# Optimization experiments

Measured on AMD Instinct MI355X. Metric: run time of the kernel, lower is better.

The kernel has to match this reference:

```python
import jax, jax.numpy as jnp
import numpy as np

HEADS, DIM_HEAD, LANDMARKS, PINV_ITERS = 8, 64, 256, 6


def moore_penrose_pinv(x, iters=PINV_ITERS):
    abs_x = jnp.abs(x)
    col = abs_x.sum(-1)
    row = abs_x.sum(-2)
    z = jnp.swapaxes(x, -1, -2) / (jnp.max(col) * jnp.max(row))
    I = jnp.eye(x.shape[-1], dtype=x.dtype)
    for _ in range(iters):
        xz = x @ z
        z = 0.25 * z @ (13 * I - xz @ (15 * I - xz @ (7 * I - xz)))
    return z


def nystrom_attention(x, w_qkv, w_out, b_out, res_conv_w):
    b, n, dim = x.shape
    m = LANDMARKS
    pad = (m - n % m) % m
    x = jnp.pad(x, ((0, 0), (pad, 0), (0, 0)))  # pad at front like F.pad(x,(0,0,pad,0))
    npad = n + pad
    qkv = x @ w_qkv  # (b, npad, 3*heads*dim_head)
    q, k, v = jnp.split(qkv, 3, axis=-1)
    sh = lambda t: t.reshape(b, npad, HEADS, DIM_HEAD).transpose(0, 2, 1, 3)
    q, k, v = sh(q), sh(k), sh(v)  # (b,h,npad,dh)
    q = q * (DIM_HEAD ** -0.5)
    l = npad // m
    q_l = q.reshape(b, HEADS, m, l, DIM_HEAD).mean(axis=3)  # landmarks (b,h,m,dh)
    k_l = k.reshape(b, HEADS, m, l, DIM_HEAD).mean(axis=3)
    attn1 = jax.nn.softmax(jnp.einsum('bhid,bhjd->bhij', q, k_l), -1)   # (b,h,npad,m)
    attn2 = jax.nn.softmax(jnp.einsum('bhid,bhjd->bhij', q_l, k_l), -1)  # (b,h,m,m)
    attn3 = jax.nn.softmax(jnp.einsum('bhid,bhjd->bhij', q_l, k), -1)   # (b,h,m,npad)
    out = attn1 @ (moore_penrose_pinv(attn2) @ (attn3 @ v))  # (b,h,npad,dh)
    # depthwise residual conv over sequence dim (Conv2d(heads,heads,(33,1),groups=heads,bias=False))
    res = jax.lax.conv_general_dilated(v, res_conv_w, (1, 1), ((16, 16), (0, 0)),
                                       dimension_numbers=('NCHW', 'OIHW', 'NCHW'),
                                       feature_group_count=HEADS)
    out = out + res
    out = out.transpose(0, 2, 1, 3).reshape(b, npad, HEADS * DIM_HEAD)
    out = out @ w_out + b_out
    return out[:, -n:]


def camil_forward(bag, adj_row, adj_col, adj_val, w_qkv, w_out, b_out, res_conv_w,
                  wq, wk, wv_w, wv_b, v_att, u_att, w_att, fc_kernel, fc_bias):
    N = bag.shape[1]
    # encoder
    xg = nystrom_attention(bag, w_qkv, w_out, b_out, res_conv_w)[0]  # (N,D)
    enc = xg + bag  # (1,N,D)
    q = enc @ wq  # (1,N,256)
    k = enc @ wk
    attn = jnp.einsum('bnd,bmd->bnm', q, k)[0] / jnp.sqrt(jnp.float32(256.0))  # (N,N)
    # sparse adjacency-masked neighbor aggregation
    edge_scores = adj_val * attn[adj_row, adj_col]
    A_raw = jax.ops.segment_sum(edge_scores, adj_row, num_segments=N)  # (N,)
    alpha = jax.nn.softmax(A_raw)
    value = bag @ wv_w + wv_b  # (1,N,D)
    xl = alpha[:, None] * value  # (1,N,D)
    wei2 = jax.nn.sigmoid(-xl) ** 2
    xo = xl * 2 * wei2 + 2 * enc * (1 - wei2)  # (1,N,D)
    # gated MIL attention (softmax over dim 0 of size 1, as in original)
    inst = jnp.tanh(xo @ v_att) * jax.nn.sigmoid(xo @ u_att)
    scores = inst @ w_att  # (1,N,1)
    k_alpha = jax.nn.softmax(scores, axis=0)
    attn_output = k_alpha * xo
    pooled = attn_output[0].sum(axis=0, keepdims=True)  # (1,D)
    out = pooled @ fc_kernel + fc_bias  # (1,1)
    return out, A_raw, k_alpha


def setup_inputs() -> dict:
    key = jax.random.key(0)
    ks = jax.random.split(key, 16)
    N, D, E = 10000, 512, 90000
    s = 0.02
    return {
        'bag': jax.random.normal(ks[0], (1, N, D), jnp.float32),
        'adj_row': jax.random.randint(ks[1], (E,), 0, N),
        'adj_col': jax.random.randint(ks[2], (E,), 0, N),
        'adj_val': jax.random.uniform(ks[3], (E,), jnp.float32),
        'w_qkv': jax.random.normal(ks[4], (D, 3 * HEADS * DIM_HEAD), jnp.float32) * s,
        'w_out': jax.random.normal(ks[5], (HEADS * DIM_HEAD, D), jnp.float32) * s,
        'b_out': jnp.zeros((D,), jnp.float32),
        'res_conv_w': jax.random.normal(ks[6], (HEADS, 1, 33, 1), jnp.float32) * s,
        'wq': jax.random.normal(ks[7], (D, 256), jnp.float32) * s,
        'wk': jax.random.normal(ks[8], (D, 256), jnp.float32) * s,
        'wv_w': jax.random.normal(ks[9], (D, D), jnp.float32) * s,
        'wv_b': jnp.zeros((D,), jnp.float32),
        'v_att': jax.random.normal(ks[10], (D, 128), jnp.float32) * s,
        'u_att': jax.random.normal(ks[11], (D, 128), jnp.float32) * s,
        'w_att': jax.random.normal(ks[12], (128, 1), jnp.float32) * s,
        'fc_kernel': jax.random.normal(ks[13], (D, 1), jnp.float32) * s,
        'fc_bias': jnp.zeros((1,), jnp.float32),
    }


def reference(bag, adj_row, adj_col, adj_val, w_qkv, w_out, b_out, res_conv_w,
              wq, wk, wv_w, wv_b, v_att, u_att, w_att, fc_kernel, fc_bias):
    return camil_forward(bag, adj_row, adj_col, adj_val, w_qkv, w_out, b_out, res_conv_w,
                         wq, wk, wv_w, wv_b, v_att, u_att, w_att, fc_kernel, fc_bias)
```

## Files before the change

### kernel.cpp

```cpp
#include <hip/hip_runtime.h>
#include <hip/hip_bf16.h>
#include <math.h>

#define NSEQ   10000
#define NPAD   10240
#define PADR   240
#define HEADS  8
#define DH     64
#define LM     256
#define LFAC   40
#define DMODEL 512
#define DQK    256
#define OUTSZ  20001
#define NSPLIT 16
#define KCH    128

typedef __attribute__((ext_vector_type(8))) short bf16x8;
typedef __attribute__((ext_vector_type(4))) float f32x4;
#define MFMA16(a,b,c) __builtin_amdgcn_mfma_f32_16x16x32_bf16(a,b,c,0,0,0)

__device__ __forceinline__ float b2f(ushort u) {
    return __uint_as_float(((unsigned)u) << 16);
}
__device__ __forceinline__ ushort f2b(float f) {
    unsigned u = __float_as_uint(f);
    unsigned r = (u + 0x7FFFu + ((u >> 16) & 1u)) >> 16;
    return (ushort)r;
}
__device__ __forceinline__ int swz8(int bid, int nwg) {
    int q = nwg >> 3, r = nwg & 7;
    int x = bid & 7, idx = bid >> 3;
    int start = (x < r) ? x * (q + 1) : r * (q + 1) + (x - r) * q;
    return start + idx;
}

__global__ __launch_bounds__(256) void cvt_k(const float* __restrict__ in,
                                             ushort* __restrict__ out, int n4)
{
    int i = blockIdx.x * 256 + threadIdx.x;
    if (i < n4) {
        float4 v = ((const float4*)in)[i];
        ushort4 u; u.x = f2b(v.x); u.y = f2b(v.y); u.z = f2b(v.z); u.w = f2b(v.w);
        ((ushort4*)out)[i] = u;
    }
}

__global__ __launch_bounds__(256)
void wtrans_k(const float* __restrict__ w_qkv, const float* __restrict__ w_out,
              const float* __restrict__ wq, const float* __restrict__ wk,
              const float* __restrict__ wv_w,
              ushort* __restrict__ wqkvT, ushort* __restrict__ woutT,
              ushort* __restrict__ wqkT)
{
    __shared__ float tile[32][33];
    int g0 = blockIdx.x * 32, r0 = blockIdx.y * 32;
    const float* in; ushort* outp; int C; int lc0;
    if (g0 < 1536)      { in = w_qkv; outp = wqkvT;                      C = 1536; lc0 = g0; }
    else if (g0 < 2048) { in = w_out; outp = woutT;                      C = 512;  lc0 = g0 - 1536; }
    else if (g0 < 2304) { in = wq;    outp = wqkT;                       C = 256;  lc0 = g0 - 2048; }
    else if (g0 < 2560) { in = wk;    outp = wqkT + 256*512;             C = 256;  lc0 = g0 - 2304; }
    else                { in = wv_w;  outp = wqkvT + (size_t)1536*512;   C = 512;  lc0 = g0 - 2560; }
    int tx = threadIdx.x & 31, ty = threadIdx.x >> 5;
    for (int i = ty; i < 32; i += 8) tile[i][tx] = in[(size_t)(r0 + i) * C + lc0 + tx];
    __syncthreads();
    for (int i = ty; i < 32; i += 8) outp[(size_t)(lc0 + i) * 512 + r0 + tx] = f2b(tile[tx][i]);
}

template<int MODE, int TN>
__global__ __launch_bounds__(256)
void mgemm(const ushort* __restrict__ A, const ushort* __restrict__ Bt,
           int Mlog, int N, int K, int padr, int nbx,
           void* __restrict__ P0, void* __restrict__ P1, void* __restrict__ P2,
           void* __restrict__ P3, void* __restrict__ P4,
           const float* __restrict__ bias, const float* __restrict__ extra)
{
    constexpr int NF = TN / 32;
    __shared__ ushort As[128 * 40];
    __shared__ ushort Bs[TN * 40];
    const int tid = threadIdx.x;
    const int l = tid & 63, w = tid >> 6;
    const int wm = w >> 1, wn = w & 1;
    const int wk_ = swz8(blockIdx.x, gridDim.x);
    const int row0 = (wk_ / nbx) * 128, col0 = (wk_ % nbx) * TN;
    const int lr = l & 15, lk = (l >> 4) * 8;
    const int lg = l >> 4;
    f32x4 acc[4][NF];
    #pragma unroll
    for (int i = 0; i < 4; ++i)
        #pragma unroll
        for (int j = 0; j < NF; ++j) acc[i][j] = (f32x4){0.f, 0.f, 0.f, 0.f};

    for (int k0 = 0; k0 < K; k0 += 32) {
        {
            int row = tid >> 1, half = (tid & 1) * 16;
            int phys = row0 + row - padr;
            uint4 v0 = {0,0,0,0}, v1 = {0,0,0,0};
            if (phys >= 0 && phys < Mlog - padr) {
                const uint4* src = (const uint4*)(A + (size_t)phys * K + k0 + half);
                v0 = src[0]; v1 = src[1];
            }
            *(uint4*)&As[row * 40 + half] = v0;
            *(uint4*)&As[row * 40 + half + 8] = v1;
        }
        if (TN == 128) {
            int row = tid >> 1, half = (tid & 1) * 16;
            const uint4* src = (const uint4*)(Bt + (size_t)(col0 + row) * K + k0 + half);
            *(uint4*)&Bs[row * 40 + half] = src[0];
            *(uint4*)&Bs[row * 40 + half + 8] = src[1];
        } else {
            int row = tid >> 2, q8 = (tid & 3) * 8;
            *(uint4*)&Bs[row * 40 + q8] =
                *(const uint4*)(Bt + (size_t)(col0 + row) * K + k0 + q8);
        }
        __syncthreads();
        bf16x8 af[4];
        #pragma unroll
        for (int mf = 0; mf < 4; ++mf)
            af[mf] = *(const bf16x8*)&As[(wm * 64 + mf * 16 + lr) * 40 + lk];
        #pragma unroll
        for (int nf = 0; nf < NF; ++nf) {
            bf16x8 bfr = *(const bf16x8*)&Bs[(wn * (TN / 2) + nf * 16 + lr) * 40 + lk];
            #pragma unroll
            for (int mf = 0; mf < 4; ++mf)
                acc[mf][nf] = MFMA16(af[mf], bfr, acc[mf][nf]);
        }
        __syncthreads();
    }

    #pragma unroll
    for (int mf = 0; mf < 4; ++mf)
    #pragma unroll
    for (int nf = 0; nf < NF; ++nf) {
        #pragma unroll
        for (int i = 0; i < 4; ++i) {
            int r = row0 + wm * 64 + mf * 16 + lg * 4 + i;
            int c = col0 + wn * (TN / 2) + nf * 16 + lr;
            float v = acc[mf][nf][i];
            if (MODE == 0) {
                int t = c >> 9;
                if (t < 3) {
                    int hh = (c >> 6) & 7, d = c & 63;
                    ushort* dst = (t == 0) ? (ushort*)P0 : (t == 1) ? (ushort*)P1 : (ushort*)P2;
                    dst[((size_t)hh * NPAD + r) * DH + d] = f2b(t == 0 ? v * 0.125f : v);
                } else {
                    int phys = r - PADR;
                    if (phys >= 0)
                        ((ushort*)P4)[(size_t)phys * DMODEL + (c & 511)] = f2b(v);
                }
            } else if (MODE == 1) {
                if (r < Mlog) {
                    float o = v + bias[c] + extra[(size_t)r * N + c];
                    ((float*)P0)[(size_t)r * N + c] = o;
                    ((ushort*)P1)[(size_t)r * N + c] = f2b(o);
                }
            } else if (MODE == 6) {
                if (r < Mlog) {
                    ushort u = f2b(v);
                    if (c < 256) ((ushort*)P0)[(size_t)r * 256 + c] = u;
                    else         ((ushort*)P1)[(size_t)r * 256 + (c - 256)] = u;
                }
            }
        }
        if (MODE == 0) {
            int c = col0 + wn * (TN / 2) + nf * 16 + lr;
            if ((c >> 9) == 2) {
                int hh = (c >> 6) & 7;
                int kt  = (row0 + wm * 64 + mf * 16 + lg * 4) >> 5;
                int lgp = ((mf * 2) + (lg >> 1)) & 3;
                int lanep = lr + lgp * 16;
                int e0 = (lg & 1) * 4;
                ushort4 pk;
                pk.x = f2b(acc[mf][nf][0]); pk.y = f2b(acc[mf][nf][1]);
                pk.z = f2b(acc[mf][nf][2]); pk.w = f2b(acc[mf][nf][3]);
                *(ushort4*)&((ushort*)P3)[(((size_t)hh * (NPAD/32) + kt) * 4 + (nf & 3)) * 512
                                          + lanep * 8 + e0] = pk;
            }
        }
    }
}

template<bool PLAIN, bool BCI>
__global__ __launch_bounds__(256)
void pinv_k(const ushort* __restrict__ A, const ushort* __restrict__ Bt,
            int N, float cval, float scale,
            ushort* __restrict__ P0, ushort* __restrict__ P1)
{
    __shared__ __align__(16) char smem[65536];
    char* As = smem;
    char* Bs = smem + 32768;
    const int tid = threadIdx.x, l = tid & 63, w = tid >> 6;
    const int wm = w >> 1, wn = w & 1;
    const int lr = l & 15, lg = l >> 4;
    const int col0 = blockIdx.x * 64, row0 = blockIdx.y * 64, h = blockIdx.z;
    const ushort* Ab = A + (size_t)h * 65536;
    const ushort* Btb = Bt + (size_t)h * ((size_t)N * 256);
    {
        int row = tid >> 2, seg = (tid & 3) * 128;
        const uint4* sa = (const uint4*)(Ab + (size_t)(row0 + row) * 256) + (tid & 3) * 8;
        const uint4* sb = (const uint4*)(Btb + (size_t)(col0 + row) * 256) + (tid & 3) * 8;
        int gn = col0 + row;
        #pragma unroll
        for (int e = 0; e < 8; ++e) {
            int off = (row * 512 + seg + e * 16) ^ ((row & 7) << 4);
            *(uint4*)(As + off) = sa[e];
            uint4 vb = sb[e];
            if (BCI) {
                union { uint4 u; ushort s[8]; } t; t.u = vb;
                int gk0 = (seg >> 1) + e * 8;
                #pragma unroll
                for (int j = 0; j < 8; ++j)
                    t.s[j] = f2b(((gn == gk0 + j) ? cval : 0.f) - b2f(t.s[j]));
                vb = t.u;
            }
            *(uint4*)(Bs + off) = vb;
        }
    }
    __syncthreads();
    f32x4 acc[2][2];
    #pragma unroll
    for (int i = 0; i < 2; ++i)
        #pragma unroll
        for (int j = 0; j < 2; ++j) acc[i][j] = (f32x4){0.f, 0.f, 0.f, 0.f};
    #pragma unroll
    for (int ks = 0; ks < 8; ++ks) {
        bf16x8 af[2], bf[2];
        #pragma unroll
        for (int mf = 0; mf < 2; ++mf) {
            int ar = wm * 32 + mf * 16 + lr;
            af[mf] = *(const bf16x8*)(As + ((ar * 512 + ks * 64 + lg * 16) ^ ((ar & 7) << 4)));
        }
        #pragma unroll
        for (int nf = 0; nf < 2; ++nf) {
            int br = wn * 32 + nf * 16 + lr;
            bf[nf] = *(const bf16x8*)(Bs + ((br * 512 + ks * 64 + lg * 16) ^ ((br & 7) << 4)));
        }
        #pragma unroll
        for (int mf = 0; mf < 2; ++mf)
            #pragma unroll
            for (int nf = 0; nf < 2; ++nf)
                acc[mf][nf] = MFMA16(af[mf], bf[nf], acc[mf][nf]);
    }
    #pragma unroll
    for (int mf = 0; mf < 2; ++mf)
    #pragma unroll
    for (int nf = 0; nf < 2; ++nf) {
        int r0v = row0 + wm * 32 + mf * 16 + lg * 4;
        int c = col0 + wn * 32 + nf * 16 + lr;
        if (PLAIN) {
            #pragma unroll
            for (int i = 0; i < 4; ++i)
                P0[(size_t)h * 256 * N + (size_t)(r0v + i) * N + c] = f2b(acc[mf][nf][i] * scale);
        }
        ushort4 pk;
        pk.x = f2b(acc[mf][nf][0] * scale); pk.y = f2b(acc[mf][nf][1] * scale);
        pk.z = f2b(acc[mf][nf][2] * scale); pk.w = f2b(acc[mf][nf][3] * scale);
        *(ushort4*)&P1[(size_t)h * ((size_t)N * 256) + (size_t)c * 256 + r0v] = pk;
    }
}

__global__ void landmark_k(const ushort* __restrict__ src, ushort* __restrict__ dst,
                           ushort* __restrict__ dstp)
{
    int b = blockIdx.x;
    int hh = b >> 8, j = b & 255, d = threadIdx.x;
    const ushort* p = src + ((size_t)hh * NPAD + (size_t)j * LFAC) * DH + d;
    float s = 0.f;
    #pragma unroll
    for (int t = 0; t < LFAC; ++t) s += b2f(p[t * DH]);
    ushort u = f2b(s * (1.f / LFAC));
    dst[((size_t)hh * LM + j) * DH + d] = u;
    if (dstp) {
        int nf = j >> 4, lr = j & 15;
        int ks = d >> 5, lg = (d >> 3) & 3, e = d & 7;
        dstp[(((size_t)hh * 16 + nf) * 2 + ks) * 512 + (lg * 16 + lr) * 8 + e] = u;
    }
}

__global__ __launch_bounds__(256)
void wpack_k(const ushort* __restrict__ WT, ushort* __restrict__ Wpk)
{
    int h = blockIdx.x;
    for (int it = 0; it < 8; ++it) {
        int idx = it * 256 + threadIdx.x;
        int nf = idx >> 9, ks = (idx >> 6) & 7, l = idx & 63;
        int lr = l & 15, lg = l >> 4;
        uint4 v = *(const uint4*)(WT + ((size_t)h * 64 + nf * 16 + lr) * 256 + ks * 32 + lg * 8);
        *(uint4*)(Wpk + ((size_t)h * 2048 + idx) * 8) = v;
    }
}

__global__ __launch_bounds__(256)
void attn2_k(const ushort* __restrict__ QL, const ushort* __restrict__ KL,
             ushort* __restrict__ X2b)
{
    int i = blockIdx.x, h = blockIdx.y, j = threadIdx.x;
    __shared__ float qv[DH];
    __shared__ float red[256];
    if (j < DH) qv[j] = b2f(QL[((size_t)h * LM + i) * DH + j]);
    __syncthreads();
    const ushort* kp = KL + ((size_t)h * LM + j) * DH;
    float dot = 0.f;
    #pragma unroll
    for (int d = 0; d < DH; ++d) dot += qv[d] * b2f(kp[d]);
    red[j] = dot; __syncthreads();
    for (int s = 128; s > 0; s >>= 1) { if (j < s) red[j] = fmaxf(red[j], red[j + s]); __syncthreads(); }
    float mx = red[0]; __syncthreads();
    float e = __expf(dot - mx);
    red[j] = e; __syncthreads();
    for (int s = 128; s > 0; s >>= 1) { if (j < s) red[j] += red[j + s]; __syncthreads(); }
    X2b[((size_t)h * LM + i) * LM + j] = f2b(e / red[0]);
}

__global__ __launch_bounds__(256)
void colrow_k(const ushort* __restrict__ X2b, unsigned int* __restrict__ mx)
{
    int h = blockIdx.x, t = threadIdx.x;
    const ushort* x = X2b + (size_t)h * LM * LM;
    float cs = 0.f, rs = 0.f;
    for (int j = 0; j < LM; ++j) cs += fabsf(b2f(x[(size_t)t * LM + j]));
    for (int i = 0; i < LM; ++i) rs += fabsf(b2f(x[(size_t)i * LM + t]));
    __shared__ float r1[256], r2[256];
    r1[t] = cs; r2[t] = rs; __syncthreads();
    for (int s = 128; s > 0; s >>= 1) {
        if (t < s) { r1[t] = fmaxf(r1[t], r1[t + s]); r2[t] = fmaxf(r2[t], r2[t + s]); }
        __syncthreads();
    }
    if (t == 0) {
        atomicMax(&mx[0], __float_as_uint(r1[0]));
        atomicMax(&mx[1], __float_as_uint(r2[0]));
    }
}

__global__ void zinit_k(const ushort* __restrict__ X2b, const float* __restrict__ mxf,
                        ushort* __restrict__ Z, ushort* __restrict__ Zt)
{
    int i = blockIdx.x, h = blockIdx.y, j = threadIdx.x;
    float scale = 1.f / (mxf[0] * mxf[1]);
    float x = b2f(X2b[((size_t)h * LM + i) * LM + j]) * scale;
    ushort u = f2b(x);
    Z[((size_t)h * LM + j) * LM + i] = u;
    Zt[((size_t)h * LM + i) * LM + j] = u;
}

__global__ __launch_bounds__(256)
void attn3_fa(const ushort* __restrict__ QLb, const ushort* __restrict__ Kb,
              const ushort* __restrict__ VtPk,
              float* __restrict__ Opart, float* __restrict__ Mpart,
              float* __restrict__ Lpart)
{
    __shared__ __align__(16) char smem[9216 + 18432];
    ushort* Qs = (ushort*)smem;
    ushort* Ks = (ushort*)(smem + 9216);
    ushort* Ps = (ushort*)(smem + 9216);
    const int tid = threadIdx.x, l = tid & 63, wv = tid >> 6;
    const int split = blockIdx.x, qt = blockIdx.y, h = blockIdx.z;
    const int lr = l & 15, lg = l >> 4;
    {
        int row = tid >> 2, seg = (tid & 3) * 16;
        const uint4* src = (const uint4*)(QLb + ((size_t)h * LM + qt * 64 + row) * DH + seg);
        *(uint4*)&Qs[row * 72 + seg] = src[0];
        *(uint4*)&Qs[row * 72 + seg + 8] = src[1];
    }
    f32x4 o[4];
    float m_[4], l_[4];
    #pragma unroll
    for (int nf = 0; nf < 4; ++nf) o[nf] = (f32x4){0.f, 0.f, 0.f, 0.f};
    #pragma unroll
    for (int i = 0; i < 4; ++i) { m_[i] = -INFINITY; l_[i] = 0.f; }
    const int k0base = split * (NPAD / NSPLIT);
    for (int ch = 0; ch < NPAD / NSPLIT / KCH; ++ch) {
        int kg0 = k0base + ch * KCH;
        __syncthreads();
        {
            int row = tid >> 1, half = (tid & 1) * 32;
            const uint4* src = (const uint4*)(Kb + ((size_t)h * NPAD + kg0 + row) * DH + half);
            #pragma unroll
            for (int e = 0; e < 4; ++e) *(uint4*)&Ks[row * 72 + half + e * 8] = src[e];
        }
        __syncthreads();
        f32x4 s[8];
        #pragma unroll
        for (int nf = 0; nf < 8; ++nf) s[nf] = (f32x4){0.f, 0.f, 0.f, 0.f};
        #pragma unroll
        for (int ks = 0; ks < 2; ++ks) {
            bf16x8 a = *(const bf16x8*)&Qs[(wv * 16 + lr) * 72 + ks * 32 + lg * 8];
            #pragma unroll
            for (int nf = 0; nf < 8; ++nf) {
                bf16x8 b = *(const bf16x8*)&Ks[(nf * 16 + lr) * 72 + ks * 32 + lg * 8];
                s[nf] = MFMA16(a, b, s[nf]);
            }
        }
        float scl[4];
        #pragma unroll
        for (int i = 0; i < 4; ++i) {
            float mx = s[0][i];
            #pragma unroll
            for (int nf = 1; nf < 8; ++nf) mx = fmaxf(mx, s[nf][i]);
            mx = fmaxf(mx, __shfl_xor(mx, 1)); mx = fmaxf(mx, __shfl_xor(mx, 2));
            mx = fmaxf(mx, __shfl_xor(mx, 4)); mx = fmaxf(mx, __shfl_xor(mx, 8));
            float mn = fmaxf(m_[i], mx);
            float sum = 0.f;
            #pragma unroll
            for (int nf = 0; nf < 8; ++nf) {
                float e = __expf(s[nf][i] - mn); s[nf][i] = e; sum += e;
            }
            sum += __shfl_xor(sum, 1); sum += __shfl_xor(sum, 2);
            sum += __shfl_xor(sum, 4); sum += __shfl_xor(sum, 8);
            float sc = __expf(m_[i] - mn);
            l_[i] = l_[i] * sc + sum;
            m_[i] = mn;
            scl[i] = sc;
        }
        #pragma unroll
        for (int nf = 0; nf < 4; ++nf)
        #pragma unroll
        for (int i = 0; i < 4; ++i) o[nf][i] *= scl[i];
        __syncthreads();
        #pragma unroll
        for (int nf = 0; nf < 8; ++nf)
        #pragma unroll
        for (int i = 0; i < 4; ++i) {
            int row = wv * 16 + lg * 4 + i;
            int col = nf * 16 + lr;
            Ps[row * 128 + (col ^ ((row & 7) << 3))] = f2b(s[nf][i]);
        }
        #pragma unroll
        for (int ks = 0; ks < 4; ++ks) {
            int row = wv * 16 + lr;
            int kcol = ks * 32 + lg * 8;
            bf16x8 a = *(const bf16x8*)&Ps[row * 128 + (kcol ^ ((row & 7) << 3))];
            int kgt = (kg0 >> 5) + ks;
            #pragma unroll
            for (int nf = 0; nf < 4; ++nf) {
                bf16x8 b = *(const bf16x8*)(VtPk +
                    (((size_t)h * (NPAD/32) + kgt) * 4 + nf) * 512 + (size_t)l * 8);
                o[nf] = MFMA16(a, b, o[nf]);
            }
        }
    }
    const int base = (split * 4 + qt) * 8 + h;
    #pragma unroll
    for (int nf = 0; nf < 4; ++nf)
    #pragma unroll
    for (int i = 0; i < 4; ++i) {
        int r = wv * 16 + lg * 4 + i;
        int c = nf * 16 + lr;
        Opart[((size_t)base * 64 + r) * 64 + c] = o[nf][i];
    }
    if (lr == 0) {
        #pragma unroll
        for (int i = 0; i < 4; ++i) {
            int r = wv * 16 + lg * 4 + i;
            Mpart[base * 64 + r] = m_[i];
            Lpart[base * 64 + r] = l_[i];
        }
    }
}

__global__ __launch_bounds__(256)
void mergeAV_k(const float* __restrict__ Opart, const float* __restrict__ Mpart,
               const float* __restrict__ Lpart, ushort* __restrict__ AVt)
{
    int qt = blockIdx.x, h = blockIdx.y, rq = blockIdx.z;
    int t = threadIdx.x;
    int r = rq * 32 + (t >> 3), c0 = (t & 7) * 8;
    float mv[NSPLIT];
    float mstar = -INFINITY;
    #pragma unroll
    for (int s = 0; s < NSPLIT; ++s) {
        mv[s] = Mpart[((s * 4 + qt) * 8 + h) * 64 + r];
        mstar = fmaxf(mstar, mv[s]);
    }
    float wgt[NSPLIT];
    float L = 0.f;
    #pragma unroll
    for (int s = 0; s < NSPLIT; ++s) {
        wgt[s] = __expf(mv[s] - mstar);
        L += wgt[s] * Lpart[((s * 4 + qt) * 8 + h) * 64 + r];
    }
    float inv = 1.f / L;
    float acc[8] = {};
    #pragma unroll
    for (int s = 0; s < NSPLIT; ++s) {
        const float* op = Opart + (((size_t)(s * 4 + qt) * 8 + h) * 64 + r) * 64 + c0;
        #pragma unroll
        for (int e = 0; e < 8; ++e) acc[e] += wgt[s] * op[e];
    }
    #pragma unroll
    for (int e = 0; e < 8; ++e)
        AVt[((size_t)h * DH + c0 + e) * LM + qt * 64 + r] = f2b(acc[e] * inv);
}

__global__ __launch_bounds__(256)
void conv_k(const ushort* __restrict__ Vb, const float* __restrict__ cw,
            ushort* __restrict__ OBc)
{
    int idx = blockIdx.x * 256 + threadIdx.x;
    if (idx >= NSEQ * 128) return;
    int ro = idx >> 7, c4 = idx & 127;
    int h = c4 >> 4, dq = (c4 & 15) * 4;
    int i = ro + PADR;
    float a0 = 0, a1 = 0, a2 = 0, a3 = 0;
    #pragma unroll
    for (int tt = 0; tt < 33; ++tt) {
        int src = i + tt - 16;
        if (src < NPAD) {
            float wv = cw[h * 33 + tt];
            ushort4 u = *(const ushort4*)(Vb + ((size_t)h * NPAD + src) * DH + dq);
            a0 += wv * b2f(u.x); a1 += wv * b2f(u.y);
            a2 += wv * b2f(u.z); a3 += wv * b2f(u.w);
        }
    }
    ushort4 o; o.x = f2b(a0); o.y = f2b(a1); o.z = f2b(a2); o.w = f2b(a3);
    *(ushort4*)&OBc[(size_t)ro * DMODEL + h * DH + dq] = o;
}

__global__ __launch_bounds__(256, 4)
void outrows64v2(const ushort* __restrict__ Qb, const ushort* __restrict__ KLpk,
                 const ushort* __restrict__ Wpk, const ushort* __restrict__ OBc,
                 ushort* __restrict__ OBb)
{
    __shared__ __align__(16) char smem[40960];
    char*   Qs  = smem;
    ushort* KLs = (ushort*)(smem + 8192);
    ushort* Ps  = (ushort*)(smem + 8192);
    const int tid = threadIdx.x, l = tid & 63, w = tid >> 6;
    const int h = blockIdx.y, i0 = blockIdx.x * 64;
    const int lr = l & 15, lg = l >> 4;

    ushort obc[4][4];
    #pragma unroll
    for (int nf = 0; nf < 4; ++nf)
    #pragma unroll
    for (int i = 0; i < 4; ++i) {
        int r = i0 + w * 16 + lg * 4 + i;
        obc[nf][i] = (r >= PADR)
            ? OBc[(size_t)(r - PADR) * DMODEL + h * DH + nf * 16 + lr] : (ushort)0;
    }
    {
        int row = tid >> 2;
        int seg = (tid & 3) * 32;
        const uint4* src = (const uint4*)(Qb + ((size_t)h * NPAD + i0 + row) * DH) + (tid & 3) * 2;
        uint4 v0 = src[0], v1 = src[1];
        int sw = (row & 7) << 4;
        *(uint4*)(Qs + row * 128 + (seg ^ sw)) = v0;
        *(uint4*)(Qs + row * 128 + ((seg + 16) ^ sw)) = v1;
    }
    {
        const uint4* src = (const uint4*)(KLpk + (size_t)h * 16384) + tid;
        uint4* dst = (uint4*)KLs + tid;
        #pragma unroll
        for (int e = 0; e < 8; ++e) dst[e * 256] = src[e * 256];
    }
    __syncthreads();

    f32x4 s[16];
    #pragma unroll
    for (int nf = 0; nf < 16; ++nf) s[nf] = (f32x4){0.f, 0.f, 0.f, 0.f};
    #pragma unroll
    for (int ks = 0; ks < 2; ++ks) {
        int qrow = w * 16 + lr;
        bf16x8 a = *(const bf16x8*)(Qs + qrow * 128 +
                                    ((ks * 64 + lg * 16) ^ ((qrow & 7) << 4)));
        #pragma unroll
        for (int nf = 0; nf < 16; ++nf) {
            bf16x8 b = *(const bf16x8*)&KLs[((nf * 2 + ks) * 64 + l) * 8];
            s[nf] = MFMA16(a, b, s[nf]);
        }
    }
    float inv_[4];
    #pragma unroll
    for (int i = 0; i < 4; ++i) {
        float m = s[0][i];
        #pragma unroll
        for (int nf = 1; nf < 16; ++nf) m = fmaxf(m, s[nf][i]);
        m = fmaxf(m, __shfl_xor(m, 1)); m = fmaxf(m, __shfl_xor(m, 2));
        m = fmaxf(m, __shfl_xor(m, 4)); m = fmaxf(m, __shfl_xor(m, 8));
        float sum = 0.f;
        #pragma unroll
        for (int nf = 0; nf < 16; ++nf) {
            float e = __expf(s[nf][i] - m); s[nf][i] = e; sum += e;
        }
        sum += __shfl_xor(sum, 1); sum += __shfl_xor(sum, 2);
        sum += __shfl_xor(sum, 4); sum += __shfl_xor(sum, 8);
        inv_[i] = 1.f / sum;
    }
    __syncthreads();
    #pragma unroll
    for (int nf = 0; nf < 16; ++nf)
    #pragma unroll
    for (int i = 0; i < 4; ++i) {
        int row = w * 16 + lg * 4 + i;
        int col = nf * 16 + lr;
        Ps[row * 256 + (col ^ ((row & 7) << 3))] = f2b(s[nf][i] * inv_[i]);
    }
    f32x4 o[4];
    #pragma unroll
    for (int nf = 0; nf < 4; ++nf) o[nf] = (f32x4){0.f, 0.f, 0.f, 0.f};
    #pragma unroll
    for (int ks = 0; ks < 8; ++ks) {
        int row = w * 16 + lr;
        int kcol = ks * 32 + lg * 8;
        bf16x8 a = *(const bf16x8*)&Ps[row * 256 + (kcol ^ ((row & 7) << 3))];
        #pragma unroll
        for (int nf = 0; nf < 4; ++nf) {
            bf16x8 b = *(const bf16x8*)(Wpk + (((size_t)h * 2048) + nf * 512 + ks * 64 + l) * 8);
            o[nf] = MFMA16(a, b, o[nf]);
        }
    }
    #pragma unroll
    for (int nf = 0; nf < 4; ++nf)
    #pragma unroll
    for (int i = 0; i < 4; ++i) {
        int r = i0 + w * 16 + lg * 4 + i;
        if (r >= PADR) {
            int ro = r - PADR;
            int c = h * DH + nf * 16 + lr;
            OBb[(size_t)ro * DMODEL + c] = f2b(o[nf][i] + b2f(obc[nf][i]));
        }
    }
}

__global__ __launch_bounds__(256)
void edges_k(const int* __restrict__ rows, const int* __restrict__ cols,
             const float* __restrict__ vals,
             const ushort* __restrict__ QE, const ushort* __restrict__ KE,
             float* __restrict__ A_raw, int E)
{
    int gid = blockIdx.x * blockDim.x + threadIdx.x;
    int e = gid >> 6, l = gid & 63;
    if (e >= E) return;
    int r = rows[e], c = cols[e];
    ushort4 qv = *(const ushort4*)(QE + (size_t)r * DQK + l * 4);
    ushort4 kv = *(const ushort4*)(KE + (size_t)c * DQK + l * 4);
    float dot = b2f(qv.x) * b2f(kv.x) + b2f(qv.y) * b2f(kv.y)
              + b2f(qv.z) * b2f(kv.z) + b2f(qv.w) * b2f(kv.w);
    #pragma unroll
    for (int s = 32; s > 0; s >>= 1) dot += __shfl_down(dot, s);
    if (l == 0) atomicAdd(&A_raw[r], vals[e] * dot * 0.0625f);
}

__global__ __launch_bounds__(1024)
void alphasm_k(const float* __restrict__ A_raw, float* __restrict__ alpha)
{
    __shared__ float red[1024];
    int t = threadIdx.x;
    float lm = -INFINITY;
    for (int i = t; i < NSEQ; i += 1024) lm = fmaxf(lm, A_raw[i]);
    red[t] = lm; __syncthreads();
    for (int s = 512; s > 0; s >>= 1) { if (t < s) red[t] = fmaxf(red[t], red[t + s]); __syncthreads(); }
    float mx = red[0]; __syncthreads();
    float ls = 0.f;
    for (int i = t; i < NSEQ; i += 1024) ls += __expf(A_raw[i] - mx);
    red[t] = ls; __syncthreads();
    for (int s = 512; s > 0; s >>= 1) { if (t < s) red[t] += red[t + s]; __syncthreads(); }
    float inv = 1.f / red[0];
    for (int i = t; i < NSEQ; i += 1024) alpha[i] = __expf(A_raw[i] - mx) * inv;
}

__global__ void init_k(float* __restrict__ out, const float* __restrict__ fcb,
                       unsigned int* __restrict__ mx)
{
    int t = blockIdx.x * blockDim.x + threadIdx.x;
    if (t == 0) { out[0] = fcb[0]; mx[0] = 0u; mx[1] = 0u; }
    if (t >= 1 && t <= NSEQ) out[t] = 0.f;
    if (t >= NSEQ + 1 && t < OUTSZ) out[t] = 1.0f;
}

__global__ __launch_bounds__(256)
void xo_pooled_k(const ushort* __restrict__ VALb, const float* __restrict__ ENCf,
                 const float* __restrict__ alpha, const float* __restrict__ wvb,
                 const float* __restrict__ fck, float* __restrict__ out0)
{
    __shared__ float red[256];
    int t = threadIdx.x;
    float acc = 0.f;
    const int total = NSEQ * 128;
    for (int idx = blockIdx.x * 256 + t; idx < total; idx += gridDim.x * 256) {
        int r = idx >> 7, dq = (idx & 127) * 4;
        float al = alpha[r];
        ushort4 v4 = *(const ushort4*)(VALb + (size_t)r * DMODEL + dq);
        float4 e4 = *(const float4*)(ENCf + (size_t)r * DMODEL + dq);
        float4 b4 = *(const float4*)(wvb + dq);
        float4 f4 = *(const float4*)(fck + dq);
        float vv[4] = {b2f(v4.x) + b4.x, b2f(v4.y) + b4.y,
                       b2f(v4.z) + b4.z, b2f(v4.w) + b4.w};
        float ee[4] = {e4.x, e4.y, e4.z, e4.w};
        float ff[4] = {f4.x, f4.y, f4.z, f4.w};
        #pragma unroll
        for (int j = 0; j < 4; ++j) {
            float xl = al * vv[j];
            float s = 1.f / (1.f + __expf(xl));
            float w2 = s * s;
            float xo = 2.f * xl * w2 + 2.f * ee[j] * (1.f - w2);
            acc += xo * ff[j];
        }
    }
    red[t] = acc; __syncthreads();
    for (int s = 128; s > 0; s >>= 1) { if (t < s) red[t] += red[t + s]; __syncthreads(); }
    if (t == 0) atomicAdd(out0, red[0]);
}

extern "C" void kernel_launch(void* const* d_in, const int* in_sizes, int n_in,
                              void* d_out, int out_size, void* d_ws, size_t ws_size,
                              hipStream_t stream)
{
    (void)n_in; (void)out_size; (void)ws_size;
    const float* bag   = (const float*)d_in[0];
    const int*   arow  = (const int*)d_in[1];
    const int*   acol  = (const int*)d_in[2];
    const float* aval  = (const float*)d_in[3];
    const float* w_qkv = (const float*)d_in[4];
    const float* w_out = (const float*)d_in[5];
    const float* b_out = (const float*)d_in[6];
    const float* convw = (const float*)d_in[7];
    const float* wq    = (const float*)d_in[8];
    const float* wk    = (const float*)d_in[9];
    const float* wv_w  = (const float*)d_in[10];
    const float* wv_b  = (const float*)d_in[11];
    const float* fck   = (const float*)d_in[15];
    const float* fcb   = (const float*)d_in[16];
    const int E = in_sizes[1];
    float* out = (float*)d_out;

    char* ws = (char*)d_ws;
    size_t off = 0;
    auto alloc = [&](size_t bytes) { void* p = ws + off; off += (bytes + 255) & ~(size_t)255; return p; };
    ushort* Qb    = (ushort*)alloc((size_t)HEADS * NPAD * DH * 2);
    ushort* Kb    = (ushort*)alloc((size_t)HEADS * NPAD * DH * 2);
    ushort* Vb    = (ushort*)alloc((size_t)HEADS * NPAD * DH * 2);
    ushort* bagb  = (ushort*)alloc((size_t)NSEQ * DMODEL * 2);
    ushort* wqkvT = (ushort*)alloc((size_t)2048 * 512 * 2);
    ushort* woutT = (ushort*)alloc((size_t)512 * 512 * 2);
    ushort* wqkT  = (ushort*)alloc((size_t)512 * 512 * 2);
    ushort* VALb  = (ushort*)alloc((size_t)NSEQ * DMODEL * 2);
    ushort* QLb   = (ushort*)alloc((size_t)HEADS * LM * DH * 2);
    ushort* KLb   = (ushort*)alloc((size_t)HEADS * LM * DH * 2);
    ushort* KLpk  = (ushort*)alloc((size_t)HEADS * LM * DH * 2);
    ushort* Wpk   = (ushort*)alloc((size_t)HEADS * DH * LM * 2);
    ushort* X2b   = (ushort*)alloc((size_t)HEADS * LM * LM * 2);
    ushort* Za    = (ushort*)alloc((size_t)HEADS * LM * LM * 2);
    ushort* Zat   = (ushort*)alloc((size_t)HEADS * LM * LM * 2);
    ushort* Zb2   = (ushort*)alloc((size_t)HEADS * LM * LM * 2);
    ushort* Zbt2  = (ushort*)alloc((size_t)HEADS * LM * LM * 2);
    ushort* T0    = (ushort*)alloc((size_t)HEADS * LM * LM * 2);
    ushort* T0t   = (ushort*)alloc((size_t)HEADS * LM * LM * 2);
    ushort* T1t   = (ushort*)alloc((size_t)HEADS * LM * LM * 2);
    ushort* T2t   = (ushort*)alloc((size_t)HEADS * LM * LM * 2);
    ushort* AVt   = (ushort*)alloc((size_t)HEADS * DH * LM * 2);
    ushort* WT    = (ushort*)alloc((size_t)HEADS * DH * LM * 2);
    ushort* OBc   = (ushort*)alloc((size_t)NSEQ * DMODEL * 2);
    ushort* OBb   = (ushort*)alloc((size_t)NSEQ * DMODEL * 2);
    float*  ENCf  = (float*)alloc((size_t)NSEQ * DMODEL * 4);
    ushort* ENCb  = (ushort*)alloc((size_t)NSEQ * DMODEL * 2);
    float*  ALPHA = (float*)alloc((size_t)NPAD * 4);
    float*  MXf   = (float*)alloc(256);
    unsigned int* MX = (unsigned int*)MXf;
    ushort* QEb = Qb;
    ushort* KEb = Kb;
    ushort* VtPk  = (ushort*)ENCf;
    float*  Opart = (float*)ENCb;
    float*  Mpart = (float*)((char*)ENCb + 8388608);
    float*  Lpart = (float*)((char*)ENCb + 8519680);

    init_k<<<(OUTSZ + 255) / 256, 256, 0, stream>>>(out, fcb, MX);

    cvt_k<<<(NSEQ * DMODEL / 4 + 255) / 256, 256, 0, stream>>>(bag, bagb, NSEQ * DMODEL / 4);
    wtrans_k<<<dim3(96, 16), 256, 0, stream>>>(w_qkv, w_out, wq, wk, wv_w,
                                               wqkvT, woutT, wqkT);

    mgemm<0, 128><<<1280, 256, 0, stream>>>(
        bagb, wqkvT, NPAD, 2048, 512, PADR, 16,
        Qb, Kb, Vb, VtPk, VALb, nullptr, nullptr);

    landmark_k<<<HEADS * LM, DH, 0, stream>>>(Qb, QLb, nullptr);
    landmark_k<<<HEADS * LM, DH, 0, stream>>>(Kb, KLb, KLpk);

    attn2_k<<<dim3(LM, HEADS), 256, 0, stream>>>(QLb, KLb, X2b);
    colrow_k<<<HEADS, 256, 0, stream>>>(X2b, MX);
    zinit_k<<<dim3(LM, HEADS), 256, 0, stream>>>(X2b, MXf, Za, Zat);

    ushort *Z = Za, *Zt = Zat, *Zn = Zb2, *Znt = Zbt2;
    for (int it = 0; it < 6; ++it) {
        pinv_k<true,  false><<<dim3(4, 4, HEADS), 256, 0, stream>>>(
            X2b, Zt, LM, 0.f, 1.f, T0, T0t);
        pinv_k<false, true ><<<dim3(4, 4, HEADS), 256, 0, stream>>>(
            T0, T0t, LM, 7.f, 1.f, nullptr, T1t);
        pinv_k<false, true ><<<dim3(4, 4, HEADS), 256, 0, stream>>>(
            T0, T1t, LM, 15.f, 1.f, nullptr, T2t);
        pinv_k<true,  true ><<<dim3(4, 4, HEADS), 256, 0, stream>>>(
            Z, T2t, LM, 13.f, 0.25f, Zn, Znt);
        ushort* t;
        t = Z; Z = Zn; Zn = t;
        t = Zt; Zt = Znt; Znt = t;
    }

    attn3_fa<<<dim3(NSPLIT, 4, HEADS), 256, 0, stream>>>(QLb, Kb, VtPk, Opart, Mpart, Lpart);
    mergeAV_k<<<dim3(4, HEADS, 2), 256, 0, stream>>>(Opart, Mpart, Lpart, AVt);
    pinv_k<false, false><<<dim3(1, 4, HEADS), 256, 0, stream>>>(
        Za, AVt, DH, 0.f, 1.f, nullptr, WT);
    wpack_k<<<HEADS, 256, 0, stream>>>(WT, Wpk);

    conv_k<<<(NSEQ * 128 + 255) / 256, 256, 0, stream>>>(Vb, convw, OBc);
    outrows64v2<<<dim3(NPAD / 64, HEADS), 256, 0, stream>>>(Qb, KLpk, Wpk, OBc, OBb);

    mgemm<1, 64><<<632, 256, 0, stream>>>(
        OBb, woutT, NSEQ, DMODEL, 512, 0, 8,
        ENCf, ENCb, nullptr, nullptr, nullptr, b_out, bag);

    mgemm<6, 64><<<632, 256, 0, stream>>>(
        ENCb, wqkT, NSEQ, 512, 512, 0, 8,
        QEb, KEb, nullptr, nullptr, nullptr, nullptr, nullptr);

    edges_k<<<(E * 64 + 255) / 256, 256, 0, stream>>>(arow, acol, aval, QEb, KEb, out + 1, E);
    alphasm_k<<<1, 1024, 0, stream>>>(out + 1, ALPHA);

    xo_pooled_k<<<1280, 256, 0, stream>>>(VALb, ENCf, ALPHA, wv_b, fck, out);
}
```

Measured before the change: 420.8 us.

## Fuse small kernels and halve pinv row tiles to double block count

The output-initialisation kernel is folded into the bf16 conversion kernel, and the two landmark-mean launches are merged into one. The weight-packing kernel is dropped by having the final pinv GEMM write its result directly in the MFMA-packed layout. The pinv GEMM tile shrinks from 64x64 to 32x64 rows per block, doubling the grid so the small 256x256 per-head products occupy more CUs. The costs are more redundant B-tile loads per output element and a hand-computed packed-layout index that has to match what the consumer expects.

```diff
diff --git a/kernel.cpp b/kernel.cpp
--- a/kernel.cpp
+++ b/kernel.cpp
@@ -34,8 +34,10 @@
     return start + idx;
 }
 
-__global__ __launch_bounds__(256) void cvt_k(const float* __restrict__ in,
-                                             ushort* __restrict__ out, int n4)
+__global__ __launch_bounds__(256)
+void cvt_k(const float* __restrict__ in, ushort* __restrict__ out, int n4,
+           float* __restrict__ outbuf, const float* __restrict__ fcb,
+           unsigned int* __restrict__ mx)
 {
     int i = blockIdx.x * 256 + threadIdx.x;
     if (i < n4) {
@@ -43,6 +45,9 @@
         ushort4 u; u.x = f2b(v.x); u.y = f2b(v.y); u.z = f2b(v.z); u.w = f2b(v.w);
         ((ushort4*)out)[i] = u;
     }
+    if (i == 0) { outbuf[0] = fcb[0]; mx[0] = 0u; mx[1] = 0u; }
+    if (i >= 1 && i <= NSEQ) outbuf[i] = 0.f;
+    if (i >= NSEQ + 1 && i < OUTSZ) outbuf[i] = 1.0f;
 }
 
 __global__ __launch_bounds__(256)
@@ -179,30 +184,36 @@
     }
 }
 
-template<bool PLAIN, bool BCI>
+template<bool PLAIN, bool BCI, bool WPK>
 __global__ __launch_bounds__(256)
 void pinv_k(const ushort* __restrict__ A, const ushort* __restrict__ Bt,
             int N, float cval, float scale,
             ushort* __restrict__ P0, ushort* __restrict__ P1)
 {
-    __shared__ __align__(16) char smem[65536];
+    __shared__ __align__(16) char smem[49152];
     char* As = smem;
-    char* Bs = smem + 32768;
+    char* Bs = smem + 16384;
     const int tid = threadIdx.x, l = tid & 63, w = tid >> 6;
-    const int wm = w >> 1, wn = w & 1;
     const int lr = l & 15, lg = l >> 4;
-    const int col0 = blockIdx.x * 64, row0 = blockIdx.y * 64, h = blockIdx.z;
+    const int col0 = blockIdx.x * 64, row0 = blockIdx.y * 32, h = blockIdx.z;
     const ushort* Ab = A + (size_t)h * 65536;
     const ushort* Btb = Bt + (size_t)h * ((size_t)N * 256);
     {
+        int row = tid >> 3, seg = (tid & 7) * 64;
+        const uint4* sa = (const uint4*)(Ab + (size_t)(row0 + row) * 256) + (tid & 7) * 4;
+        #pragma unroll
+        for (int e = 0; e < 4; ++e) {
+            int off = (row * 512 + seg + e * 16) ^ ((row & 7) << 4);
+            *(uint4*)(As + off) = sa[e];
+        }
+    }
+    {
         int row = tid >> 2, seg = (tid & 3) * 128;
-        const uint4* sa = (const uint4*)(Ab + (size_t)(row0 + row) * 256) + (tid & 3) * 8;
         const uint4* sb = (const uint4*)(Btb + (size_t)(col0 + row) * 256) + (tid & 3) * 8;
         int gn = col0 + row;
         #pragma unroll
         for (int e = 0; e < 8; ++e) {
             int off = (row * 512 + seg + e * 16) ^ ((row & 7) << 4);
-            *(uint4*)(As + off) = sa[e];
             uint4 vb = sb[e];
             if (BCI) {
                 union { uint4 u; ushort s[8]; } t; t.u = vb;
@@ -216,76 +227,62 @@
         }
     }
     __syncthreads();
-    f32x4 acc[2][2];
-    #pragma unroll
-    for (int i = 0; i < 2; ++i)
-        #pragma unroll
-        for (int j = 0; j < 2; ++j) acc[i][j] = (f32x4){0.f, 0.f, 0.f, 0.f};
+    f32x4 acc[2];
+    acc[0] = (f32x4){0.f, 0.f, 0.f, 0.f};
+    acc[1] = (f32x4){0.f, 0.f, 0.f, 0.f};
     #pragma unroll
     for (int ks = 0; ks < 8; ++ks) {
-        bf16x8 af[2], bf[2];
+        bf16x8 af[2];
         #pragma unroll
         for (int mf = 0; mf < 2; ++mf) {
-            int ar = wm * 32 + mf * 16 + lr;
+            int ar = mf * 16 + lr;
             af[mf] = *(const bf16x8*)(As + ((ar * 512 + ks * 64 + lg * 16) ^ ((ar & 7) << 4)));
         }
-        #pragma unroll
-        for (int nf = 0; nf < 2; ++nf) {
-            int br = wn * 32 + nf * 16 + lr;
-            bf[nf] = *(const bf16x8*)(Bs + ((br * 512 + ks * 64 + lg * 16) ^ ((br & 7) << 4)));
-        }
-        #pragma unroll
-        for (int mf = 0; mf < 2; ++mf)
-            #pragma unroll
-            for (int nf = 0; nf < 2; ++nf)
-                acc[mf][nf] = MFMA16(af[mf], bf[nf], acc[mf][nf]);
-    }
-    #pragma unroll
-    for (int mf = 0; mf < 2; ++mf)
-    #pragma unroll
-    for (int nf = 0; nf < 2; ++nf) {
-        int r0v = row0 + wm * 32 + mf * 16 + lg * 4;
-        int c = col0 + wn * 32 + nf * 16 + lr;
+        int br = w * 16 + lr;
+        bf16x8 bf = *(const bf16x8*)(Bs + ((br * 512 + ks * 64 + lg * 16) ^ ((br & 7) << 4)));
+        acc[0] = MFMA16(af[0], bf, acc[0]);
+        acc[1] = MFMA16(af[1], bf, acc[1]);
+    }
+    #pragma unroll
+    for (int mf = 0; mf < 2; ++mf) {
+        int r0v = row0 + mf * 16 + lg * 4;
+        int c = col0 + w * 16 + lr;
         if (PLAIN) {
             #pragma unroll
             for (int i = 0; i < 4; ++i)
-                P0[(size_t)h * 256 * N + (size_t)(r0v + i) * N + c] = f2b(acc[mf][nf][i] * scale);
+                P0[(size_t)h * 256 * N + (size_t)(r0v + i) * N + c] = f2b(acc[mf][i] * scale);
         }
         ushort4 pk;
-        pk.x = f2b(acc[mf][nf][0] * scale); pk.y = f2b(acc[mf][nf][1] * scale);
-        pk.z = f2b(acc[mf][nf][2] * scale); pk.w = f2b(acc[mf][nf][3] * scale);
-        *(ushort4*)&P1[(size_t)h * ((size_t)N * 256) + (size_t)c * 256 + r0v] = pk;
-    }
-}
-
-__global__ void landmark_k(const ushort* __restrict__ src, ushort* __restrict__ dst,
-                           ushort* __restrict__ dstp)
+        pk.x = f2b(acc[mf][0] * scale); pk.y = f2b(acc[mf][1] * scale);
+        pk.z = f2b(acc[mf][2] * scale); pk.w = f2b(acc[mf][3] * scale);
+        if (WPK) {
+            int off = (((c >> 4) * 8 + (r0v >> 5)) << 9) + (((r0v >> 3) & 3) << 7)
+                    + ((c & 15) << 3) + (r0v & 4);
+            *(ushort4*)&P1[(size_t)h * 16384 + off] = pk;
+        } else {
+            *(ushort4*)&P1[(size_t)h * ((size_t)N * 256) + (size_t)c * 256 + r0v] = pk;
+        }
+    }
+}
+
+__global__ void landmark2_k(const ushort* __restrict__ Qb, const ushort* __restrict__ Kb,
+                            ushort* __restrict__ QLb, ushort* __restrict__ KLb,
+                            ushort* __restrict__ KLpk)
 {
     int b = blockIdx.x;
+    bool isK = b >= HEADS * LM;
+    if (isK) b -= HEADS * LM;
     int hh = b >> 8, j = b & 255, d = threadIdx.x;
-    const ushort* p = src + ((size_t)hh * NPAD + (size_t)j * LFAC) * DH + d;
+    const ushort* p = (isK ? Kb : Qb) + ((size_t)hh * NPAD + (size_t)j * LFAC) * DH + d;
     float s = 0.f;
     #pragma unroll
     for (int t = 0; t < LFAC; ++t) s += b2f(p[t * DH]);
     ushort u = f2b(s * (1.f / LFAC));
-    dst[((size_t)hh * LM + j) * DH + d] = u;
-    if (dstp) {
+    (isK ? KLb : QLb)[((size_t)hh * LM + j) * DH + d] = u;
+    if (isK) {
         int nf = j >> 4, lr = j & 15;
         int ks = d >> 5, lg = (d >> 3) & 3, e = d & 7;
-        dstp[(((size_t)hh * 16 + nf) * 2 + ks) * 512 + (lg * 16 + lr) * 8 + e] = u;
-    }
-}
-
-__global__ __launch_bounds__(256)
-void wpack_k(const ushort* __restrict__ WT, ushort* __restrict__ Wpk)
-{
-    int h = blockIdx.x;
-    for (int it = 0; it < 8; ++it) {
-        int idx = it * 256 + threadIdx.x;
-        int nf = idx >> 9, ks = (idx >> 6) & 7, l = idx & 63;
-        int lr = l & 15, lg = l >> 4;
-        uint4 v = *(const uint4*)(WT + ((size_t)h * 64 + nf * 16 + lr) * 256 + ks * 32 + lg * 8);
-        *(uint4*)(Wpk + ((size_t)h * 2048 + idx) * 8) = v;
+        KLpk[(((size_t)hh * 16 + nf) * 2 + ks) * 512 + (lg * 16 + lr) * 8 + e] = u;
     }
 }
 
@@ -656,15 +653,6 @@
     for (int s = 512; s > 0; s >>= 1) { if (t < s) red[t] += red[t + s]; __syncthreads(); }
     float inv = 1.f / red[0];
     for (int i = t; i < NSEQ; i += 1024) alpha[i] = __expf(A_raw[i] - mx) * inv;
-}
-
-__global__ void init_k(float* __restrict__ out, const float* __restrict__ fcb,
-                       unsigned int* __restrict__ mx)
-{
-    int t = blockIdx.x * blockDim.x + threadIdx.x;
-    if (t == 0) { out[0] = fcb[0]; mx[0] = 0u; mx[1] = 0u; }
-    if (t >= 1 && t <= NSEQ) out[t] = 0.f;
-    if (t >= NSEQ + 1 && t < OUTSZ) out[t] = 1.0f;
 }
 
 __global__ __launch_bounds__(256)
@@ -748,7 +736,6 @@
     ushort* T1t   = (ushort*)alloc((size_t)HEADS * LM * LM * 2);
     ushort* T2t   = (ushort*)alloc((size_t)HEADS * LM * LM * 2);
     ushort* AVt   = (ushort*)alloc((size_t)HEADS * DH * LM * 2);
-    ushort* WT    = (ushort*)alloc((size_t)HEADS * DH * LM * 2);
     ushort* OBc   = (ushort*)alloc((size_t)NSEQ * DMODEL * 2);
     ushort* OBb   = (ushort*)alloc((size_t)NSEQ * DMODEL * 2);
     float*  ENCf  = (float*)alloc((size_t)NSEQ * DMODEL * 4);
@@ -763,9 +750,8 @@
     float*  Mpart = (float*)((char*)ENCb + 8388608);
     float*  Lpart = (float*)((char*)ENCb + 8519680);
 
-    init_k<<<(OUTSZ + 255) / 256, 256, 0, stream>>>(out, fcb, MX);
-
-    cvt_k<<<(NSEQ * DMODEL / 4 + 255) / 256, 256, 0, stream>>>(bag, bagb, NSEQ * DMODEL / 4);
+    cvt_k<<<(NSEQ * DMODEL / 4 + 255) / 256, 256, 0, stream>>>(
+        bag, bagb, NSEQ * DMODEL / 4, out, fcb, MX);
     wtrans_k<<<dim3(96, 16), 256, 0, stream>>>(w_qkv, w_out, wq, wk, wv_w,
                                                wqkvT, woutT, wqkT);
 
@@ -773,8 +759,7 @@
         bagb, wqkvT, NPAD, 2048, 512, PADR, 16,
         Qb, Kb, Vb, VtPk, VALb, nullptr, nullptr);
 
-    landmark_k<<<HEADS * LM, DH, 0, stream>>>(Qb, QLb, nullptr);
-    landmark_k<<<HEADS * LM, DH, 0, stream>>>(Kb, KLb, KLpk);
+    landmark2_k<<<2 * HEADS * LM, DH, 0, stream>>>(Qb, Kb, QLb, KLb, KLpk);
 
     attn2_k<<<dim3(LM, HEADS), 256, 0, stream>>>(QLb, KLb, X2b);
     colrow_k<<<HEADS, 256, 0, stream>>>(X2b, MX);
@@ -782,13 +767,13 @@
 
     ushort *Z = Za, *Zt = Zat, *Zn = Zb2, *Znt = Zbt2;
     for (int it = 0; it < 6; ++it) {
-        pinv_k<true,  false><<<dim3(4, 4, HEADS), 256, 0, stream>>>(
+        pinv_k<true,  false, false><<<dim3(4, 8, HEADS), 256, 0, stream>>>(
             X2b, Zt, LM, 0.f, 1.f, T0, T0t);
-        pinv_k<false, true ><<<dim3(4, 4, HEADS), 256, 0, stream>>>(
+        pinv_k<false, true,  false><<<dim3(4, 8, HEADS), 256, 0, stream>>>(
             T0, T0t, LM, 7.f, 1.f, nullptr, T1t);
-        pinv_k<false, true ><<<dim3(4, 4, HEADS), 256, 0, stream>>>(
+        pinv_k<false, true,  false><<<dim3(4, 8, HEADS), 256, 0, stream>>>(
             T0, T1t, LM, 15.f, 1.f, nullptr, T2t);
-        pinv_k<true,  true ><<<dim3(4, 4, HEADS), 256, 0, stream>>>(
+        pinv_k<true,  true,  false><<<dim3(4, 8, HEADS), 256, 0, stream>>>(
             Z, T2t, LM, 13.f, 0.25f, Zn, Znt);
         ushort* t;
         t = Z; Z = Zn; Zn = t;
@@ -797,9 +782,8 @@
 
     attn3_fa<<<dim3(NSPLIT, 4, HEADS), 256, 0, stream>>>(QLb, Kb, VtPk, Opart, Mpart, Lpart);
     mergeAV_k<<<dim3(4, HEADS, 2), 256, 0, stream>>>(Opart, Mpart, Lpart, AVt);
-    pinv_k<false, false><<<dim3(1, 4, HEADS), 256, 0, stream>>>(
-        Za, AVt, DH, 0.f, 1.f, nullptr, WT);
-    wpack_k<<<HEADS, 256, 0, stream>>>(WT, Wpk);
+    pinv_k<false, false, true><<<dim3(1, 8, HEADS), 256, 0, stream>>>(
+        Za, AVt, DH, 0.f, 1.f, nullptr, Wpk);
 
     conv_k<<<(NSEQ * 128 + 255) / 256, 256, 0, stream>>>(Vb, convw, OBc);
     outrows64v2<<<dim3(NPAD / 64, HEADS), 256, 0, stream>>>(Qb, KLpk, Wpk, OBc, OBb);
```

New measurement: 376.9 us. 1.12x faster.
